# Performance work log

Hardware: AMD Instinct MI355X
Metric: run time of the kernel (lower is better)

The kernel has to match this reference:

```python
import jax, jax.numpy as jnp
import numpy as np
from jax import lax

WSIZE = 11
SIGMA = 1.5
PAD = WSIZE // 2  # 5
C1 = 0.01 ** 2
C2 = 0.03 ** 2


def _gauss1d():
    x = np.arange(WSIZE) - WSIZE // 2
    g = np.exp(-(x.astype(np.float64) ** 2) / (2.0 * SIGMA ** 2))
    g = g / g.sum()
    return jnp.asarray(g, dtype=jnp.float32)


def _blur3d(x, g):
    """Replicate-pad by 5 on D/H/W then apply the separable 11x11x11 Gaussian.
    x: [N, 1, D, H, W]. Mathematically identical to the dense conv3d in the
    original (the 3D window is an exact outer product of the 1D Gaussian)."""
    xp = jnp.pad(x, ((0, 0), (0, 0), (PAD, PAD), (PAD, PAD), (PAD, PAD)), mode='edge')
    dn = ('NCDHW', 'OIDHW', 'NCDHW')
    for kshape in ((1, 1, WSIZE, 1, 1), (1, 1, 1, WSIZE, 1), (1, 1, 1, 1, WSIZE)):
        xp = lax.conv_general_dilated(xp, g.reshape(kshape), (1, 1, 1), 'VALID',
                                      dimension_numbers=dn)
    return xp


def _rerange(img):
    img = jnp.where(img.max() > 128.0, img / 255.0, img)
    img = jnp.where(img.min() < -0.5, (img + 1.0) / 2.0, img)
    return img


def setup_inputs() -> dict:
    key = jax.random.key(0)
    k1, k2 = jax.random.split(key)
    N, C, H, W = 4, 16, 512, 512
    pred = jax.random.uniform(k1, (N, C, H, W), dtype=jnp.float32)
    gt = jax.random.uniform(k2, (N, C, H, W), dtype=jnp.float32)
    return {"pred": pred, "gt": gt}


def reference(pred, gt):
    N = pred.shape[0]
    pred = _rerange(pred)
    gt = _rerange(gt)

    # ---- PSNR (range = 1.0, reduce='sum') ----
    mse = jnp.mean((pred - gt) ** 2, axis=(1, 2, 3))           # [N]
    psnr = jnp.sum(10.0 * jnp.log10(1.0 / mse))                # scalar

    # ---- 3D SSIM over [N,1,C,H,W] volumes ----
    g = _gauss1d()
    img = pred[:, None]                                        # [N,1,D,H,W]
    gtt = gt[:, None]
    mu1 = _blur3d(img, g)
    mu2 = _blur3d(gtt, g)
    mu1_sq = mu1 * mu1
    mu2_sq = mu2 * mu2
    mu1_mu2 = mu1 * mu2
    sigma1_sq = _blur3d(img * img, g) - mu1_sq
    sigma2_sq = _blur3d(gtt * gtt, g) - mu2_sq
    sigma12 = _blur3d(img * gtt, g) - mu1_mu2

    v1 = 2.0 * sigma12 + C2
    v2 = sigma1_sq + sigma2_sq + C2
    ssim_map = ((2.0 * mu1_mu2 + C1) * v1) / ((mu1_sq + mu2_sq + C1) * v2)
    ssim = jnp.sum(jnp.mean(ssim_map, axis=(1, 2, 3, 4)))      # reduce='sum'

    return psnr, ssim, N
```

## Files before the change

kernel.cpp:

```cpp
#include <hip/hip_runtime.h>
#include <cmath>


#define NB 4
#define DD 16
#define HH 512
#define WW 512
#define SLICE (HH * WW)
#define VOL (DD * SLICE)
#define C1F 0.0001f
#define C2F 0.0009f

#define TH 16
#define TW 32
#define SW 42
#define RP 13
#define CP 21
#define CPP 22
#define CPT 22
#define NTHR 512
#define SIT (RP * SW)
#define HIT (TH * CP)
#define XTRA (SIT - NTHR)

typedef _Float16 h2v __attribute__((ext_vector_type(2)));

struct KArg {
  float wlT[DD * DD];
  unsigned ge[6], go[6];
};

__device__ inline float dot2h(unsigned a, unsigned b, float c) {
#if __has_builtin(__builtin_amdgcn_fdot2)
  return __builtin_amdgcn_fdot2(__builtin_bit_cast(h2v, a),
                                __builtin_bit_cast(h2v, b), c, false);
#else
  h2v av = __builtin_bit_cast(h2v, a), bv = __builtin_bit_cast(h2v, b);
  return fmaf((float)av.y, (float)bv.y, fmaf((float)av.x, (float)bv.x, c));
#endif
}
__device__ inline unsigned pkh(float a, float b) {
  return __builtin_bit_cast(unsigned, __builtin_amdgcn_cvt_pkrtz(a, b));
}
__device__ inline int iclamp(int v, int lo, int hi) {
  return v < lo ? lo : (v > hi ? hi : v);
}

__device__ inline float block_sum512(float v) {
#pragma unroll
  for (int o = 32; o > 0; o >>= 1) v += __shfl_down(v, o, 64);
  __shared__ float r[8];
  if ((threadIdx.x & 63) == 0) r[threadIdx.x >> 6] = v;
  __syncthreads();
  float out = 0.f;
  if (threadIdx.x == 0) {
#pragma unroll
    for (int i = 0; i < 8; ++i) out += r[i];
  }
  __syncthreads();
  return out;
}

__global__ void zero_acc_k(float* acc) {
  if (threadIdx.x < 8) acc[threadIdx.x] = 0.f;
}

__global__ __launch_bounds__(NTHR, 2) void fused_k(
    const float* __restrict__ pred, const float* __restrict__ gt,
    float* __restrict__ acc, KArg ka) {
  __shared__ uint2 sA[2][RP * 2 * CPP];
  __shared__ uint2 sB[2][RP * 2 * CPP];
  __shared__ uint2 tA[TH * CPT];
  __shared__ uint2 tB[TH * CPT];

  int b = blockIdx.x;
  int tile = b & 511;
  int n = b >> 9;
  int th0 = (tile >> 4) * TH;
  int tw0 = (tile & 15) * TW;
  int t = threadIdx.x;

  int rpA = t / SW, xA = t - rpA * SW;
  int r0A = th0 + 2 * rpA - 5;
  int gxA = iclamp(tw0 + xA - 5, 0, WW - 1);
  int go00 = iclamp(r0A, 0, HH - 1) * WW + gxA;
  int go01 = iclamp(r0A + 1, 0, HH - 1) * WW + gxA;
  int wof0 = (rpA * 2 + (xA & 1)) * CPP + (xA >> 1);
  bool oxA = (xA >= 5) && (xA < 5 + TW);
  float o00 = (oxA && rpA >= 3 && rpA <= 10) ? 1.f : 0.f;
  float o01 = (oxA && rpA >= 2 && rpA <= 9) ? 1.f : 0.f;

  int i1 = t + XTRA;
  bool has2 = (i1 >= NTHR);
  int rpB = i1 / SW, xB = i1 - rpB * SW;
  int r0B = th0 + 2 * rpB - 5;
  int gxB = iclamp(tw0 + xB - 5, 0, WW - 1);
  int go10 = iclamp(r0B, 0, HH - 1) * WW + gxB;
  int go11 = iclamp(r0B + 1, 0, HH - 1) * WW + gxB;
  int wof1 = (rpB * 2 + (xB & 1)) * CPP + (xB >> 1);
  bool oxB = (xB >= 5) && (xB < 5 + TW);
  float o10 = (oxB && rpB >= 3 && rpB <= 10) ? 1.f : 0.f;
  float o11 = (oxB && rpB >= 2 && rpB <= 9) ? 1.f : 0.f;

  bool hasH = (t < HIT);
  int hr = t / CP, hcp = t - hr * CP;
  int hbase = (hr >> 1) * (2 * CPP) + hcp;
  int htad = hr * CPT + hcp;

  int wy = t >> 5, wx = t & 31;
  int wbase = wy * CPT + (wx >> 1);

  unsigned ch[6], cw[6];
#pragma unroll
  for (int j = 0; j < 6; ++j) {
    ch[j] = (hr & 1) ? ka.go[j] : ka.ge[j];
    cw[j] = (wx & 1) ? ka.go[j] : ka.ge[j];
  }

  const float* pb = pred + (size_t)n * VOL;
  const float* qb = gt + (size_t)n * VOL;

  float p00 = pb[go00], q00 = qb[go00], p01 = pb[go01], q01 = qb[go01];
  float p10 = 0.f, q10 = 0.f, p11 = 0.f, q11 = 0.f;
  if (has2) { p10 = pb[go10]; q10 = qb[go10]; p11 = pb[go11]; q11 = qb[go11]; }

  float psnr = 0.f;
  float a0[DD], a1[DD], a2[DD], a3[DD];
#pragma unroll
  for (int j = 0; j < DD; ++j) { a0[j] = a1[j] = a2[j] = a3[j] = 0.f; }

#pragma unroll 1
  for (int d = 0; d < DD; ++d) {
    uint2* sAb = sA[d & 1];
    uint2* sBb = sB[d & 1];
    {
      float S0 = p00 + q00, D0 = p00 - q00;
      float S1 = p01 + q01, D1 = p01 - q01;
      float dd0 = D0 * D0, dd1 = D1 * D1;
      psnr = fmaf(o00, dd0, psnr);
      psnr = fmaf(o01, dd1, psnr);
      sAb[wof0] = make_uint2(pkh(S0, S1), pkh(D0, D1));
      sBb[wof0] = make_uint2(pkh(S0 * S0, S1 * S1), pkh(dd0, dd1));
    }
    if (has2) {
      float S0 = p10 + q10, D0 = p10 - q10;
      float S1 = p11 + q11, D1 = p11 - q11;
      float dd0 = D0 * D0, dd1 = D1 * D1;
      psnr = fmaf(o10, dd0, psnr);
      psnr = fmaf(o11, dd1, psnr);
      sAb[wof1] = make_uint2(pkh(S0, S1), pkh(D0, D1));
      sBb[wof1] = make_uint2(pkh(S0 * S0, S1 * S1), pkh(dd0, dd1));
    }
    __syncthreads();

    if (d < DD - 1) {
      const float* pd = pb + (size_t)(d + 1) * SLICE;
      const float* qd = qb + (size_t)(d + 1) * SLICE;
      p00 = pd[go00]; q00 = qd[go00]; p01 = pd[go01]; q01 = qd[go01];
      if (has2) { p10 = pd[go10]; q10 = qd[go10]; p11 = pd[go11]; q11 = qd[go11]; }
    }

    if (hasH) {
      float e0 = 0.f, e1 = 0.f, e2 = 0.f, e3 = 0.f;
      float f0 = 0.f, f1 = 0.f, f2 = 0.f, f3 = 0.f;
#pragma unroll
      for (int j = 0; j < 6; ++j) {
        uint2 va0 = sAb[hbase + j * (2 * CPP)];
        uint2 va1 = sAb[hbase + j * (2 * CPP) + CPP];
        uint2 vb0 = sBb[hbase + j * (2 * CPP)];
        uint2 vb1 = sBb[hbase + j * (2 * CPP) + CPP];
        unsigned c = ch[j];
        e0 = dot2h(c, va0.x, e0); e1 = dot2h(c, va0.y, e1);
        f0 = dot2h(c, va1.x, f0); f1 = dot2h(c, va1.y, f1);
        e2 = dot2h(c, vb0.x, e2); e3 = dot2h(c, vb0.y, e3);
        f2 = dot2h(c, vb1.x, f2); f3 = dot2h(c, vb1.y, f3);
      }
      tA[htad] = make_uint2(pkh(e0, f0), pkh(e1, f1));
      tB[htad] = make_uint2(pkh(e2, f2), pkh(e3, f3));
    }
    __syncthreads();

    float w0 = 0.f, w1 = 0.f, w2 = 0.f, w3 = 0.f;
#pragma unroll
    for (int j = 0; j < 6; ++j) {
      uint2 va = tA[wbase + j];
      uint2 vb = tB[wbase + j];
      unsigned c = cw[j];
      w0 = dot2h(c, va.x, w0);
      w1 = dot2h(c, va.y, w1);
      w2 = dot2h(c, vb.x, w2);
      w3 = dot2h(c, vb.y, w3);
    }
    const float* wl = ka.wlT + d * DD;
#pragma unroll
    for (int dout = 0; dout < DD; ++dout) {
      float w = wl[dout];
      a0[dout] = fmaf(w, w0, a0[dout]);
      a1[dout] = fmaf(w, w1, a1[dout]);
      a2[dout] = fmaf(w, w2, a2[dout]);
      a3[dout] = fmaf(w, w3, a3[dout]);
    }
  }

  float ssum = 0.f;
#pragma unroll
  for (int j = 0; j < DD; ++j) {
    float Sb = a0[j], Db = a1[j], B1 = a2[j], B2 = a3[j];
    float SS = Sb * Sb, DDm = Db * Db;
    float m12_2 = (SS - DDm) * 0.5f;
    float msq   = (SS + DDm) * 0.5f;
    float Epq   = (B1 - B2) * 0.25f;
    float Esum  = (B1 + B2) * 0.5f;
    float sig12_2 = 2.f * Epq - m12_2;
    float svar    = Esum - msq;
    float num = (m12_2 + C1F) * (sig12_2 + C2F);
    float den = (msq + C1F) * (svar + C2F);
    ssum += num / den;
  }
  float bs = block_sum512(ssum);
  if (t == 0) atomicAdd(&acc[4 + n], bs);
  float bp = block_sum512(psnr);
  if (t == 0) atomicAdd(&acc[n], bp);
}

__global__ void final_k(const float* __restrict__ acc, float* __restrict__ out) {
  if (threadIdx.x == 0 && blockIdx.x == 0) {
    double psnr = 0.0, ssim = 0.0;
    for (int n = 0; n < NB; ++n) {
      double mse = (double)acc[n] / (double)VOL;
      psnr += 10.0 * log10(1.0 / mse);
      ssim += (double)acc[4 + n] / (double)VOL;
    }
    out[0] = (float)psnr;
    out[1] = (float)ssim;
    out[2] = (float)NB;
  }
}

static unsigned short f2h(float f) {
  union { float f; unsigned u; } v; v.f = f;
  unsigned u = v.u;
  unsigned s = (u >> 16) & 0x8000u;
  int e = (int)((u >> 23) & 0xff) - 127 + 15;
  unsigned m = u & 0x7fffffu;
  if (e <= 0) return (unsigned short)s;
  if (e >= 31) return (unsigned short)(s | 0x7c00u);
  unsigned h = ((unsigned)e << 10) | (m >> 13);
  unsigned rem = m & 0x1fffu;
  if (rem > 0x1000u || (rem == 0x1000u && (h & 1u))) h++;
  return (unsigned short)(s | h);
}

extern "C" void kernel_launch(void* const* d_in, const int* in_sizes, int n_in,
                              void* d_out, int out_size, void* d_ws, size_t ws_size,
                              hipStream_t stream) {
  const float* pred = (const float*)d_in[0];
  const float* gt = (const float*)d_in[1];
  float* acc = (float*)d_ws;

  double tt[11], s = 0.0;
  for (int i = 0; i < 11; ++i) {
    double x = i - 5;
    tt[i] = exp(-(x * x) / 4.5);
    s += tt[i];
  }
  float g[11];
  for (int i = 0; i < 11; ++i) g[i] = (float)(tt[i] / s);

  KArg ka;
  for (int dout = 0; dout < DD; ++dout) {
    for (int d = 0; d < DD; ++d) {
      float w = 0.f;
      for (int k = 0; k < 11; ++k) {
        int j = dout + k - 5;
        j = j < 0 ? 0 : (j > 15 ? 15 : j);
        if (j == d) w += g[k];
      }
      ka.wlT[d * DD + dout] = w;
    }
  }
  for (int j = 0; j < 5; ++j)
    ka.ge[j] = (unsigned)f2h(g[2 * j]) | ((unsigned)f2h(g[2 * j + 1]) << 16);
  ka.ge[5] = (unsigned)f2h(g[10]);
  ka.go[0] = ((unsigned)f2h(g[0])) << 16;
  for (int j = 1; j < 6; ++j)
    ka.go[j] = (unsigned)f2h(g[2 * j - 1]) | ((unsigned)f2h(g[2 * j]) << 16);

  zero_acc_k<<<1, 64, 0, stream>>>(acc);
  fused_k<<<NB * 512, NTHR, 0, stream>>>(pred, gt, acc, ka);
  final_k<<<1, 1, 0, stream>>>(acc, (float*)d_out);
}
```

Before: 281.7 us.

## Process depth slices in pairs, defer depth blur to packed fp16 dot products

The main loop now handles two depth slices per iteration and interleaves them in shared memory as uint4 records. The horizontal pass computes both even and odd row outputs per thread. Instead of keeping 64 float accumulators for the depth blur, each thread stores per-slice results as packed fp16 pairs and applies the depth weights at the end with fdot2. This cuts register pressure so launch bounds can rise from 2 to 4 blocks and halves the number of barriers. The host renormalizes the fp16 Gaussian weights to sum to one, which adds fp16 rounding in the depth stage that could affect accuracy.

```diff
diff --git a/kernel.cpp b/kernel.cpp
--- a/kernel.cpp
+++ b/kernel.cpp
@@ -13,21 +13,22 @@
 
 #define TH 16
 #define TW 32
-#define SW 42
-#define RP 13
-#define CP 21
-#define CPP 22
-#define CPT 22
+#define SCOLS 42
+#define NRP 13
+#define PW 22
+#define PLSTR (2 * PW)
+#define SDSL (NRP * PLSTR)
+#define TMSL (TH * PW)
 #define NTHR 512
-#define SIT (RP * SW)
-#define HIT (TH * CP)
+#define SIT (NRP * SCOLS)
 #define XTRA (SIT - NTHR)
+#define HITEMS 168
 
 typedef _Float16 h2v __attribute__((ext_vector_type(2)));
 
 struct KArg {
-  float wlT[DD * DD];
   unsigned ge[6], go[6];
+  unsigned w2[128];
 };
 
 __device__ inline float dot2h(unsigned a, unsigned b, float c) {
@@ -65,13 +66,11 @@
   if (threadIdx.x < 8) acc[threadIdx.x] = 0.f;
 }
 
-__global__ __launch_bounds__(NTHR, 2) void fused_k(
+__global__ __launch_bounds__(NTHR, 4) void fused_k(
     const float* __restrict__ pred, const float* __restrict__ gt,
     float* __restrict__ acc, KArg ka) {
-  __shared__ uint2 sA[2][RP * 2 * CPP];
-  __shared__ uint2 sB[2][RP * 2 * CPP];
-  __shared__ uint2 tA[TH * CPT];
-  __shared__ uint2 tB[TH * CPT];
+  __shared__ uint4 sd[2 * SDSL];
+  __shared__ uint4 tmp[2 * TMSL];
 
   int b = blockIdx.x;
   int tile = b & 511;
@@ -80,137 +79,156 @@
   int tw0 = (tile & 15) * TW;
   int t = threadIdx.x;
 
-  int rpA = t / SW, xA = t - rpA * SW;
-  int r0A = th0 + 2 * rpA - 5;
-  int gxA = iclamp(tw0 + xA - 5, 0, WW - 1);
-  int go00 = iclamp(r0A, 0, HH - 1) * WW + gxA;
-  int go01 = iclamp(r0A + 1, 0, HH - 1) * WW + gxA;
-  int wof0 = (rpA * 2 + (xA & 1)) * CPP + (xA >> 1);
-  bool oxA = (xA >= 5) && (xA < 5 + TW);
-  float o00 = (oxA && rpA >= 3 && rpA <= 10) ? 1.f : 0.f;
-  float o01 = (oxA && rpA >= 2 && rpA <= 9) ? 1.f : 0.f;
-
+  int rp0 = t / SCOLS, x0 = t - rp0 * SCOLS;
+  int gx0 = iclamp(tw0 + x0 - 5, 0, WW - 1);
+  int go0a = iclamp(th0 + 2 * rp0 - 5, 0, HH - 1) * WW + gx0;
+  int go0b = iclamp(th0 + 2 * rp0 - 4, 0, HH - 1) * WW + gx0;
+  int w0i = (rp0 * 2 + (x0 & 1)) * PW + (x0 >> 1);
+  bool ox0 = (x0 >= 5) && (x0 < 5 + TW);
+  float o0a = (ox0 && rp0 >= 3 && rp0 <= 10) ? 1.f : 0.f;
+  float o0b = (ox0 && rp0 >= 2 && rp0 <= 9) ? 1.f : 0.f;
   int i1 = t + XTRA;
   bool has2 = (i1 >= NTHR);
-  int rpB = i1 / SW, xB = i1 - rpB * SW;
-  int r0B = th0 + 2 * rpB - 5;
-  int gxB = iclamp(tw0 + xB - 5, 0, WW - 1);
-  int go10 = iclamp(r0B, 0, HH - 1) * WW + gxB;
-  int go11 = iclamp(r0B + 1, 0, HH - 1) * WW + gxB;
-  int wof1 = (rpB * 2 + (xB & 1)) * CPP + (xB >> 1);
-  bool oxB = (xB >= 5) && (xB < 5 + TW);
-  float o10 = (oxB && rpB >= 3 && rpB <= 10) ? 1.f : 0.f;
-  float o11 = (oxB && rpB >= 2 && rpB <= 9) ? 1.f : 0.f;
-
-  bool hasH = (t < HIT);
-  int hr = t / CP, hcp = t - hr * CP;
-  int hbase = (hr >> 1) * (2 * CPP) + hcp;
-  int htad = hr * CPT + hcp;
-
-  int wy = t >> 5, wx = t & 31;
-  int wbase = wy * CPT + (wx >> 1);
-
-  unsigned ch[6], cw[6];
-#pragma unroll
-  for (int j = 0; j < 6; ++j) {
-    ch[j] = (hr & 1) ? ka.go[j] : ka.ge[j];
-    cw[j] = (wx & 1) ? ka.go[j] : ka.ge[j];
-  }
+  int rp1 = i1 / SCOLS, x1 = i1 - rp1 * SCOLS;
+  int gx1 = iclamp(tw0 + x1 - 5, 0, WW - 1);
+  int go1a = iclamp(th0 + 2 * rp1 - 5, 0, HH - 1) * WW + gx1;
+  int go1b = iclamp(th0 + 2 * rp1 - 4, 0, HH - 1) * WW + gx1;
+  int w1i = (rp1 * 2 + (x1 & 1)) * PW + (x1 >> 1);
+  bool ox1 = (x1 >= 5) && (x1 < 5 + TW);
+  float o1a = (ox1 && rp1 >= 3 && rp1 <= 10) ? 1.f : 0.f;
+  float o1b = (ox1 && rp1 >= 2 && rp1 <= 9) ? 1.f : 0.f;
+
+  bool hasH = (t < 2 * HITEMS);
+  int hs = (t >= HITEMS) ? 1 : 0;
+  int hi = t - hs * HITEMS;
+  int hcp = hi >> 3, hm = hi & 7;
+  int hrd = hs * SDSL + hm * PLSTR + hcp;
+  int hwr = hs * TMSL + (hm * 2) * PW + hcp;
+
+  int wv = t >> 6, wl_ = t & 63;
+  int wpar = __builtin_amdgcn_readfirstlane(wv & 1);
+  int wy = (wv >> 1) * 4 + (wl_ >> 4);
+  int wxh = wl_ & 15;
+  int wrd = wy * PW + wxh;
+  unsigned cw[6];
+#pragma unroll
+  for (int J = 0; J < 6; ++J) cw[J] = wpar ? ka.go[J] : ka.ge[J];
 
   const float* pb = pred + (size_t)n * VOL;
   const float* qb = gt + (size_t)n * VOL;
 
-  float p00 = pb[go00], q00 = qb[go00], p01 = pb[go01], q01 = qb[go01];
-  float p10 = 0.f, q10 = 0.f, p11 = 0.f, q11 = 0.f;
-  if (has2) { p10 = pb[go10]; q10 = qb[go10]; p11 = pb[go11]; q11 = qb[go11]; }
-
   float psnr = 0.f;
-  float a0[DD], a1[DD], a2[DD], a3[DD];
-#pragma unroll
-  for (int j = 0; j < DD; ++j) { a0[j] = a1[j] = a2[j] = a3[j] = 0.f; }
-
-#pragma unroll 1
-  for (int d = 0; d < DD; ++d) {
-    uint2* sAb = sA[d & 1];
-    uint2* sBb = sB[d & 1];
+  unsigned h0[8], h1[8], h2[8], h3[8];
+  float LA[8], LB[8];
+
+  {
+    LA[0] = pb[go0a]; LA[1] = pb[go0b]; LA[2] = qb[go0a]; LA[3] = qb[go0b];
+    LA[4] = pb[SLICE + go0a]; LA[5] = pb[SLICE + go0b];
+    LA[6] = qb[SLICE + go0a]; LA[7] = qb[SLICE + go0b];
+    if (has2) {
+      LB[0] = pb[go1a]; LB[1] = pb[go1b]; LB[2] = qb[go1a]; LB[3] = qb[go1b];
+      LB[4] = pb[SLICE + go1a]; LB[5] = pb[SLICE + go1b];
+      LB[6] = qb[SLICE + go1a]; LB[7] = qb[SLICE + go1b];
+    }
+  }
+
+#pragma unroll
+  for (int it = 0; it < 8; ++it) {
     {
-      float S0 = p00 + q00, D0 = p00 - q00;
-      float S1 = p01 + q01, D1 = p01 - q01;
-      float dd0 = D0 * D0, dd1 = D1 * D1;
-      psnr = fmaf(o00, dd0, psnr);
-      psnr = fmaf(o01, dd1, psnr);
-      sAb[wof0] = make_uint2(pkh(S0, S1), pkh(D0, D1));
-      sBb[wof0] = make_uint2(pkh(S0 * S0, S1 * S1), pkh(dd0, dd1));
+      float SA = LA[0] + LA[2], DA = LA[0] - LA[2];
+      float SB = LA[1] + LA[3], DB = LA[1] - LA[3];
+      float dA = DA * DA, dB = DB * DB;
+      psnr = fmaf(o0a, dA, psnr); psnr = fmaf(o0b, dB, psnr);
+      sd[w0i] = make_uint4(pkh(SA, SB), pkh(DA, DB), pkh(SA * SA, SB * SB), pkh(dA, dB));
+      SA = LA[4] + LA[6]; DA = LA[4] - LA[6];
+      SB = LA[5] + LA[7]; DB = LA[5] - LA[7];
+      dA = DA * DA; dB = DB * DB;
+      psnr = fmaf(o0a, dA, psnr); psnr = fmaf(o0b, dB, psnr);
+      sd[SDSL + w0i] = make_uint4(pkh(SA, SB), pkh(DA, DB), pkh(SA * SA, SB * SB), pkh(dA, dB));
     }
     if (has2) {
-      float S0 = p10 + q10, D0 = p10 - q10;
-      float S1 = p11 + q11, D1 = p11 - q11;
-      float dd0 = D0 * D0, dd1 = D1 * D1;
-      psnr = fmaf(o10, dd0, psnr);
-      psnr = fmaf(o11, dd1, psnr);
-      sAb[wof1] = make_uint2(pkh(S0, S1), pkh(D0, D1));
-      sBb[wof1] = make_uint2(pkh(S0 * S0, S1 * S1), pkh(dd0, dd1));
+      float SA = LB[0] + LB[2], DA = LB[0] - LB[2];
+      float SB = LB[1] + LB[3], DB = LB[1] - LB[3];
+      float dA = DA * DA, dB = DB * DB;
+      psnr = fmaf(o1a, dA, psnr); psnr = fmaf(o1b, dB, psnr);
+      sd[w1i] = make_uint4(pkh(SA, SB), pkh(DA, DB), pkh(SA * SA, SB * SB), pkh(dA, dB));
+      SA = LB[4] + LB[6]; DA = LB[4] - LB[6];
+      SB = LB[5] + LB[7]; DB = LB[5] - LB[7];
+      dA = DA * DA; dB = DB * DB;
+      psnr = fmaf(o1a, dA, psnr); psnr = fmaf(o1b, dB, psnr);
+      sd[SDSL + w1i] = make_uint4(pkh(SA, SB), pkh(DA, DB), pkh(SA * SA, SB * SB), pkh(dA, dB));
     }
     __syncthreads();
 
-    if (d < DD - 1) {
-      const float* pd = pb + (size_t)(d + 1) * SLICE;
-      const float* qd = qb + (size_t)(d + 1) * SLICE;
-      p00 = pd[go00]; q00 = qd[go00]; p01 = pd[go01]; q01 = qd[go01];
-      if (has2) { p10 = pd[go10]; q10 = qd[go10]; p11 = pd[go11]; q11 = qd[go11]; }
+    if (it < 7) {
+      const float* P = pb + (size_t)(2 * it + 2) * SLICE;
+      const float* Q = qb + (size_t)(2 * it + 2) * SLICE;
+      LA[0] = P[go0a]; LA[1] = P[go0b]; LA[2] = Q[go0a]; LA[3] = Q[go0b];
+      LA[4] = P[SLICE + go0a]; LA[5] = P[SLICE + go0b];
+      LA[6] = Q[SLICE + go0a]; LA[7] = Q[SLICE + go0b];
+      if (has2) {
+        LB[0] = P[go1a]; LB[1] = P[go1b]; LB[2] = Q[go1a]; LB[3] = Q[go1b];
+        LB[4] = P[SLICE + go1a]; LB[5] = P[SLICE + go1b];
+        LB[6] = Q[SLICE + go1a]; LB[7] = Q[SLICE + go1b];
+      }
     }
 
     if (hasH) {
-      float e0 = 0.f, e1 = 0.f, e2 = 0.f, e3 = 0.f;
-      float f0 = 0.f, f1 = 0.f, f2 = 0.f, f3 = 0.f;
-#pragma unroll
-      for (int j = 0; j < 6; ++j) {
-        uint2 va0 = sAb[hbase + j * (2 * CPP)];
-        uint2 va1 = sAb[hbase + j * (2 * CPP) + CPP];
-        uint2 vb0 = sBb[hbase + j * (2 * CPP)];
-        uint2 vb1 = sBb[hbase + j * (2 * CPP) + CPP];
-        unsigned c = ch[j];
-        e0 = dot2h(c, va0.x, e0); e1 = dot2h(c, va0.y, e1);
-        f0 = dot2h(c, va1.x, f0); f1 = dot2h(c, va1.y, f1);
-        e2 = dot2h(c, vb0.x, e2); e3 = dot2h(c, vb0.y, e3);
-        f2 = dot2h(c, vb1.x, f2); f3 = dot2h(c, vb1.y, f3);
+      float pE0[4] = {0,0,0,0}, pE1[4] = {0,0,0,0};
+      float pO0[4] = {0,0,0,0}, pO1[4] = {0,0,0,0};
+#pragma unroll
+      for (int J = 0; J < 6; ++J) {
+        uint4 ve = sd[hrd + J * PLSTR];
+        uint4 vo = sd[hrd + J * PLSTR + PW];
+        unsigned cge = ka.ge[J], cgo = ka.go[J];
+        pE0[0] = dot2h(cge, ve.x, pE0[0]); pE0[1] = dot2h(cge, ve.y, pE0[1]);
+        pE0[2] = dot2h(cge, ve.z, pE0[2]); pE0[3] = dot2h(cge, ve.w, pE0[3]);
+        pE1[0] = dot2h(cgo, ve.x, pE1[0]); pE1[1] = dot2h(cgo, ve.y, pE1[1]);
+        pE1[2] = dot2h(cgo, ve.z, pE1[2]); pE1[3] = dot2h(cgo, ve.w, pE1[3]);
+        pO0[0] = dot2h(cge, vo.x, pO0[0]); pO0[1] = dot2h(cge, vo.y, pO0[1]);
+        pO0[2] = dot2h(cge, vo.z, pO0[2]); pO0[3] = dot2h(cge, vo.w, pO0[3]);
+        pO1[0] = dot2h(cgo, vo.x, pO1[0]); pO1[1] = dot2h(cgo, vo.y, pO1[1]);
+        pO1[2] = dot2h(cgo, vo.z, pO1[2]); pO1[3] = dot2h(cgo, vo.w, pO1[3]);
       }
-      tA[htad] = make_uint2(pkh(e0, f0), pkh(e1, f1));
-      tB[htad] = make_uint2(pkh(e2, f2), pkh(e3, f3));
+      tmp[hwr] = make_uint4(pkh(pE0[0], pO0[0]), pkh(pE0[1], pO0[1]),
+                            pkh(pE0[2], pO0[2]), pkh(pE0[3], pO0[3]));
+      tmp[hwr + PW] = make_uint4(pkh(pE1[0], pO1[0]), pkh(pE1[1], pO1[1]),
+                                 pkh(pE1[2], pO1[2]), pkh(pE1[3], pO1[3]));
     }
     __syncthreads();
 
-    float w0 = 0.f, w1 = 0.f, w2 = 0.f, w3 = 0.f;
-#pragma unroll
-    for (int j = 0; j < 6; ++j) {
-      uint2 va = tA[wbase + j];
-      uint2 vb = tB[wbase + j];
-      unsigned c = cw[j];
-      w0 = dot2h(c, va.x, w0);
-      w1 = dot2h(c, va.y, w1);
-      w2 = dot2h(c, vb.x, w2);
-      w3 = dot2h(c, vb.y, w3);
-    }
-    const float* wl = ka.wlT + d * DD;
-#pragma unroll
-    for (int dout = 0; dout < DD; ++dout) {
-      float w = wl[dout];
-      a0[dout] = fmaf(w, w0, a0[dout]);
-      a1[dout] = fmaf(w, w1, a1[dout]);
-      a2[dout] = fmaf(w, w2, a2[dout]);
-      a3[dout] = fmaf(w, w3, a3[dout]);
-    }
+    float wE[4] = {0,0,0,0}, wO[4] = {0,0,0,0};
+#pragma unroll
+    for (int J = 0; J < 6; ++J) {
+      uint4 v = tmp[wrd + J];
+      wE[0] = dot2h(cw[J], v.x, wE[0]); wE[1] = dot2h(cw[J], v.y, wE[1]);
+      wE[2] = dot2h(cw[J], v.z, wE[2]); wE[3] = dot2h(cw[J], v.w, wE[3]);
+    }
+#pragma unroll
+    for (int J = 0; J < 6; ++J) {
+      uint4 v = tmp[TMSL + wrd + J];
+      wO[0] = dot2h(cw[J], v.x, wO[0]); wO[1] = dot2h(cw[J], v.y, wO[1]);
+      wO[2] = dot2h(cw[J], v.z, wO[2]); wO[3] = dot2h(cw[J], v.w, wO[3]);
+    }
+    h0[it] = pkh(wE[0], wO[0]); h1[it] = pkh(wE[1], wO[1]);
+    h2[it] = pkh(wE[2], wO[2]); h3[it] = pkh(wE[3], wO[3]);
   }
 
   float ssum = 0.f;
 #pragma unroll
-  for (int j = 0; j < DD; ++j) {
-    float Sb = a0[j], Db = a1[j], B1 = a2[j], B2 = a3[j];
-    float SS = Sb * Sb, DDm = Db * Db;
+  for (int o = 0; o < DD; ++o) {
+    float A0 = 0.f, A1 = 0.f, A2 = 0.f, A3 = 0.f;
+#pragma unroll
+    for (int m = 0; m < 8; ++m) {
+      unsigned c = ka.w2[o * 8 + m];
+      A0 = dot2h(c, h0[m], A0); A1 = dot2h(c, h1[m], A1);
+      A2 = dot2h(c, h2[m], A2); A3 = dot2h(c, h3[m], A3);
+    }
+    float SS = A0 * A0, DDm = A1 * A1;
     float m12_2 = (SS - DDm) * 0.5f;
     float msq   = (SS + DDm) * 0.5f;
-    float Epq   = (B1 - B2) * 0.25f;
-    float Esum  = (B1 + B2) * 0.5f;
+    float Epq   = (A2 - A3) * 0.25f;
+    float Esum  = (A2 + A3) * 0.5f;
     float sig12_2 = 2.f * Epq - m12_2;
     float svar    = Esum - msq;
     float num = (m12_2 + C1F) * (sig12_2 + C2F);
@@ -250,6 +268,13 @@
   if (rem > 0x1000u || (rem == 0x1000u && (h & 1u))) h++;
   return (unsigned short)(s | h);
 }
+static float h2f(unsigned short h) {
+  unsigned se = (h >> 10) & 0x1f, m = h & 0x3ffu, s = ((unsigned)h & 0x8000u) << 16;
+  union { unsigned u; float f; } v;
+  if (se == 0) { v.u = s; return v.f; }
+  v.u = s | ((se - 15 + 127) << 23) | (m << 13);
+  return v.f;
+}
 
 extern "C" void kernel_launch(void* const* d_in, const int* in_sizes, int n_in,
                               void* d_out, int out_size, void* d_ws, size_t ws_size,
@@ -267,24 +292,48 @@
   float g[11];
   for (int i = 0; i < 11; ++i) g[i] = (float)(tt[i] / s);
 
+  unsigned short hg[11];
+  for (int i = 0; i < 11; ++i) hg[i] = f2h(g[i]);
+  for (int pass = 0; pass < 3; ++pass) {
+    double sum = 0.0;
+    for (int i = 0; i < 11; ++i) sum += (double)h2f(hg[i]);
+    hg[5] = f2h((float)((double)h2f(hg[5]) + (1.0 - sum)));
+  }
+
   KArg ka;
-  for (int dout = 0; dout < DD; ++dout) {
+  for (int j = 0; j < 5; ++j)
+    ka.ge[j] = (unsigned)hg[2 * j] | ((unsigned)hg[2 * j + 1] << 16);
+  ka.ge[5] = (unsigned)hg[10];
+  ka.go[0] = ((unsigned)hg[0]) << 16;
+  for (int j = 1; j < 6; ++j)
+    ka.go[j] = (unsigned)hg[2 * j - 1] | ((unsigned)hg[2 * j] << 16);
+
+  float wl[DD][DD];
+  for (int o = 0; o < DD; ++o)
     for (int d = 0; d < DD; ++d) {
       float w = 0.f;
       for (int k = 0; k < 11; ++k) {
-        int j = dout + k - 5;
+        int j = o + k - 5;
         j = j < 0 ? 0 : (j > 15 ? 15 : j);
         if (j == d) w += g[k];
       }
-      ka.wlT[d * DD + dout] = w;
-    }
-  }
-  for (int j = 0; j < 5; ++j)
-    ka.ge[j] = (unsigned)f2h(g[2 * j]) | ((unsigned)f2h(g[2 * j + 1]) << 16);
-  ka.ge[5] = (unsigned)f2h(g[10]);
-  ka.go[0] = ((unsigned)f2h(g[0])) << 16;
-  for (int j = 1; j < 6; ++j)
-    ka.go[j] = (unsigned)f2h(g[2 * j - 1]) | ((unsigned)f2h(g[2 * j]) << 16);
+      wl[d][o] = w;
+    }
+  for (int o = 0; o < DD; ++o) {
+    unsigned short wv[DD];
+    int dmx = 0;
+    for (int d = 0; d < DD; ++d) {
+      wv[d] = f2h(wl[d][o]);
+      if (wl[d][o] > wl[dmx][o]) dmx = d;
+    }
+    for (int pass = 0; pass < 3; ++pass) {
+      double sum = 0.0;
+      for (int d = 0; d < DD; ++d) sum += (double)h2f(wv[d]);
+      wv[dmx] = f2h((float)((double)h2f(wv[dmx]) + (1.0 - sum)));
+    }
+    for (int m = 0; m < 8; ++m)
+      ka.w2[o * 8 + m] = (unsigned)wv[2 * m] | ((unsigned)wv[2 * m + 1] << 16);
+  }
 
   zero_acc_k<<<1, 64, 0, stream>>>(acc);
   fused_k<<<NB * 512, NTHR, 0, stream>>>(pred, gt, acc, ka);
```

Measured after the change: 576.9 us. 105% more time.
